# Kernel optimization log

Measured on AMD Instinct MI355X. Metric: run time of the kernel, lower is better.

Reference implementation:

```python
import jax, jax.numpy as jnp
import numpy as np

N, E, DIM, H = 50000, 800000, 64, 4

def setup_inputs() -> dict:
    key = jax.random.key(0)
    k0, k1, k2, k3, k4 = jax.random.split(key, 5)
    h_v = jax.random.normal(k0, (N, DIM), dtype=jnp.float32)
    src = jax.random.randint(k1, (E,), 0, N, dtype=jnp.int64)
    dst = jax.random.randint(k2, (E,), 0, N, dtype=jnp.int64)
    W_fc = jax.random.normal(k3, (DIM * H, DIM), dtype=jnp.float32) * 0.05
    b_fc = jnp.zeros((DIM * H,), dtype=jnp.float32)
    W_pi = jax.random.normal(k4, (1, DIM * H), dtype=jnp.float32) * 0.05
    return {"h_v": h_v, "src": src, "dst": dst, "W_fc": W_fc, "b_fc": b_fc, "W_pi": W_pi}

def reference(h_v, src, dst, W_fc, b_fc, W_pi):
    n, dim = h_v.shape
    heads = W_fc.shape[0] // dim
    # fc: [N, dim] -> [N, H*dim]
    ft = h_v @ W_fc.T + b_fc
    # u_mul_v: per-edge elementwise product of src/dst features  [E, H*dim]
    e = ft[src] * ft[dst]
    # pi + LeakyReLU(0.2): per-edge scalar score  [E]
    s = jax.nn.leaky_relu(e @ W_pi.T, negative_slope=0.2)[:, 0]
    # edge_softmax over incoming edges of each destination node (stable)
    smax = jax.ops.segment_max(s, dst, num_segments=n)
    ex = jnp.exp(s - smax[dst])
    denom = jax.ops.segment_sum(ex, dst, num_segments=n)
    a = ex / denom[dst]                        # [E]
    # u_mul_e + scatter-sum into destination nodes  [N, H*dim]
    agg = jax.ops.segment_sum(ft[src] * a[:, None], dst, num_segments=n)
    # max-pool over heads  [N, dim]
    return agg.reshape(n, heads, dim).max(axis=1)
```

## Files before the change

kernel.cpp:

```cpp
#include <hip/hip_runtime.h>
#include <math.h>

#define DIM 64
#define FDIM 256
#define MAXD 64
#define DEFER_THR 4.0f
#define XSTR 20

typedef _Float16 h2 __attribute__((ext_vector_type(2)));
typedef float f2 __attribute__((ext_vector_type(2)));

__global__ __launch_bounds__(256) void fc_kernel(const float* __restrict__ h,
                                                 const float* __restrict__ W,
                                                 const float* __restrict__ b,
                                                 _Float16* __restrict__ ft,
                                                 int* __restrict__ cnt, int N)
{
    for (int i = blockIdx.x * blockDim.x + threadIdx.x; i < N;
         i += gridDim.x * blockDim.x) cnt[i] = 0;

    int t = threadIdx.x;
    float w[DIM];
#pragma unroll
    for (int j = 0; j < DIM / 4; ++j) {
        float4 v = *(const float4*)(W + (size_t)t * DIM + j * 4);
        w[4 * j + 0] = v.x; w[4 * j + 1] = v.y;
        w[4 * j + 2] = v.z; w[4 * j + 3] = v.w;
    }
    float bt = b[t];
    for (int r = blockIdx.x; r < N; r += gridDim.x) {
        const float4* h4 = (const float4*)(h + (size_t)r * DIM);
        float acc = bt;
#pragma unroll
        for (int j = 0; j < DIM / 4; ++j) {
            float4 hv = h4[j];
            acc = fmaf(hv.x, w[4 * j + 0], acc);
            acc = fmaf(hv.y, w[4 * j + 1], acc);
            acc = fmaf(hv.z, w[4 * j + 2], acc);
            acc = fmaf(hv.w, w[4 * j + 3], acc);
        }
        ft[(size_t)r * FDIM + t] = (_Float16)acc;
    }
}

__global__ void bucket_kernel(const int* __restrict__ src, const int* __restrict__ dst,
                              int* __restrict__ cnt, unsigned short* __restrict__ egrid,
                              int E)
{
    int i = blockIdx.x * blockDim.x + threadIdx.x;
    if (i < E) {
        int d = dst[i];
        int slot = atomicAdd(&cnt[d], 1);
        egrid[(size_t)d * MAXD + slot] = (unsigned short)src[i];
    }
}

__global__ __launch_bounds__(256) void agg_kernel(const _Float16* __restrict__ ft,
                                                  const int* __restrict__ cnt,
                                                  const unsigned short* __restrict__ egrid,
                                                  const float* __restrict__ Wpi,
                                                  float* __restrict__ out, int N)
{
    __shared__ float xb[4][64 * XSTR];
    int wid = (blockIdx.x * blockDim.x + threadIdx.x) >> 6;
    int wv  = threadIdx.x >> 6;
    int lane = threadIdx.x & 63;
    if (wid >= N) return;
    int q  = lane >> 4;
    int ql = lane & 15;

    h2 fdwh[8];
    {
        const float* wp = Wpi + ql * 16;
        const _Float16* drow = ft + (size_t)wid * FDIM + ql * 16;
        uint4 a = *(const uint4*)(drow);
        uint4 b = *(const uint4*)(drow + 8);
        const h2* da = (const h2*)&a;
        const h2* db = (const h2*)&b;
#pragma unroll
        for (int j = 0; j < 4; ++j) {
            h2 v = da[j], u = db[j];
            fdwh[j].x     = (_Float16)((float)v.x * wp[2 * j + 0]);
            fdwh[j].y     = (_Float16)((float)v.y * wp[2 * j + 1]);
            fdwh[4 + j].x = (_Float16)((float)u.x * wp[8 + 2 * j + 0]);
            fdwh[4 + j].y = (_Float16)((float)u.y * wp[8 + 2 * j + 1]);
        }
    }

    int e0 = wid * MAXD;
    int e1 = e0 + cnt[wid];
    float mq = -INFINITY, lq = 0.f;
    f2 acc2[8];
#pragma unroll
    for (int j = 0; j < 8; ++j) acc2[j] = (f2){0.f, 0.f};

    auto IDX = [&](int it, int& s1, int& s2, bool& v1, bool& v2) {
        int lo = e0 + it * 8 + q, hi = e0 + it * 8 + q + 4;
        v1 = lo < e1; v2 = hi < e1;
        s1 = egrid[v1 ? lo : e0];
        s2 = egrid[v2 ? hi : e0];
    };
    auto ROWS = [&](int s1, int s2, uint4& a1, uint4& b1, uint4& a2, uint4& b2) {
        const _Float16* r1 = ft + (size_t)s1 * FDIM + ql * 16;
        const _Float16* r2 = ft + (size_t)s2 * FDIM + ql * 16;
        a1 = *(const uint4*)(r1);
        b1 = *(const uint4*)(r1 + 8);
        a2 = *(const uint4*)(r2);
        b2 = *(const uint4*)(r2 + 8);
    };
    auto COMP8 = [&](uint4 a1, uint4 b1, uint4 a2, uint4 b2, bool v1, bool v2) {
        const h2* fa1 = (const h2*)&a1; const h2* fb1 = (const h2*)&b1;
        const h2* fa2 = (const h2*)&a2; const h2* fb2 = (const h2*)&b2;
        float p1 = 0.f, p2 = 0.f;
#pragma unroll
        for (int j = 0; j < 4; ++j) {
            p1 = __builtin_amdgcn_fdot2(fa1[j], fdwh[j], p1, false);
            p2 = __builtin_amdgcn_fdot2(fa2[j], fdwh[j], p2, false);
        }
#pragma unroll
        for (int j = 0; j < 4; ++j) {
            p1 = __builtin_amdgcn_fdot2(fb1[j], fdwh[4 + j], p1, false);
            p2 = __builtin_amdgcn_fdot2(fb2[j], fdwh[4 + j], p2, false);
        }
        p1 += __shfl_xor(p1, 1, 64);  p2 += __shfl_xor(p2, 1, 64);
        p1 += __shfl_xor(p1, 2, 64);  p2 += __shfl_xor(p2, 2, 64);
        p1 += __shfl_xor(p1, 4, 64);  p2 += __shfl_xor(p2, 4, 64);
        p1 += __shfl_xor(p1, 8, 64);  p2 += __shfl_xor(p2, 8, 64);
        float s1 = p1 > 0.f ? p1 : 0.2f * p1;
        float s2 = p2 > 0.f ? p2 : 0.2f * p2;
        if (!v1) s1 = -INFINITY;
        if (!v2) s2 = -INFINITY;
        float smax = fmaxf(s1, s2);
        if (smax > mq + DEFER_THR) {
            float sc = __expf(mq - smax);
            lq *= sc;
            f2 sc2 = {sc, sc};
#pragma unroll
            for (int j = 0; j < 8; ++j) acc2[j] *= sc2;
            mq = smax;
        }
        float pe1 = v1 ? __expf(s1 - mq) : 0.f;
        float pe2 = v2 ? __expf(s2 - mq) : 0.f;
        lq += pe1 + pe2;
        f2 pe1v = {pe1, pe1}, pe2v = {pe2, pe2};
#pragma unroll
        for (int j = 0; j < 4; ++j) {
            f2 w1 = {(float)fa1[j].x, (float)fa1[j].y};
            f2 w2 = {(float)fa2[j].x, (float)fa2[j].y};
            acc2[j] = __builtin_elementwise_fma(pe1v, w1,
                       __builtin_elementwise_fma(pe2v, w2, acc2[j]));
            f2 u1 = {(float)fb1[j].x, (float)fb1[j].y};
            f2 u2 = {(float)fb2[j].x, (float)fb2[j].y};
            acc2[4 + j] = __builtin_elementwise_fma(pe1v, u1,
                           __builtin_elementwise_fma(pe2v, u2, acc2[4 + j]));
        }
    };

    if (e0 < e1) {
        int nit = (e1 - e0 + 7) >> 3;
        int iAs1, iAs2, iBs1, iBs2, iCs1, iCs2;
        bool vA1, vA2, vB1, vB2, vC1, vC2;
        uint4 Ra1, Rb1, Ra2, Rb2, Sa1, Sb1, Sa2, Sb2;
        IDX(0, iAs1, iAs2, vA1, vA2);
        if (nit > 1) IDX(1, iBs1, iBs2, vB1, vB2);
        ROWS(iAs1, iAs2, Ra1, Rb1, Ra2, Rb2);
        int it = 0;
        while (true) {
            if (it + 2 < nit) IDX(it + 2, iCs1, iCs2, vC1, vC2);
            if (it + 1 < nit) ROWS(iBs1, iBs2, Sa1, Sb1, Sa2, Sb2);
            COMP8(Ra1, Rb1, Ra2, Rb2, vA1, vA2);
            ++it; if (it >= nit) break;
            iAs1 = iBs1; iAs2 = iBs2; vA1 = vB1; vA2 = vB2;
            iBs1 = iCs1; iBs2 = iCs2; vB1 = vC1; vB2 = vC2;
            if (it + 2 < nit) IDX(it + 2, iCs1, iCs2, vC1, vC2);
            if (it + 1 < nit) ROWS(iBs1, iBs2, Ra1, Rb1, Ra2, Rb2);
            COMP8(Sa1, Sb1, Sa2, Sb2, vA1, vA2);
            ++it; if (it >= nit) break;
            iAs1 = iBs1; iAs2 = iBs2; vA1 = vB1; vA2 = vB2;
            iBs1 = iCs1; iBs2 = iCs2; vB1 = vC1; vB2 = vC2;
        }
    }

    float mstar = fmaxf(mq, __shfl_xor(mq, 16, 64));
    mstar = fmaxf(mstar, __shfl_xor(mstar, 32, 64));
    float sc = (lq > 0.f) ? __expf(mq - mstar) : 0.f;
    float lt = lq * sc;
    lt += __shfl_xor(lt, 16, 64);
    lt += __shfl_xor(lt, 32, 64);
    float inv = (lt > 0.f) ? 1.f / lt : 0.f;

    {
        float* wp = &xb[wv][(unsigned)lane * XSTR];
        f2 sc2 = {sc, sc};
#pragma unroll
        for (int k = 0; k < 4; ++k) {
            f2 lo = acc2[2 * k] * sc2;
            f2 hi = acc2[2 * k + 1] * sc2;
            *(float4*)(wp + 4 * k) = make_float4(lo.x, lo.y, hi.x, hi.y);
        }
    }
    asm volatile("s_waitcnt lgkmcnt(0)" ::: "memory");
    {
        int col = lane >> 4, jp = lane & 15;
        float A[4];
#pragma unroll
        for (int h = 0; h < 4; ++h) {
            int rowb = (col + 4 * h) * XSTR + jp;
            float v0 = xb[wv][rowb];
            float v1 = xb[wv][rowb + 16 * XSTR];
            float v2 = xb[wv][rowb + 32 * XSTR];
            float v3 = xb[wv][rowb + 48 * XSTR];
            A[h] = (v0 + v1) + (v2 + v3);
        }
        float r = fmaxf(fmaxf(A[0], A[1]), fmaxf(A[2], A[3])) * inv;
        out[(size_t)wid * DIM + lane] = r;
    }
}

extern "C" void kernel_launch(void* const* d_in, const int* in_sizes, int n_in,
                              void* d_out, int out_size, void* d_ws, size_t ws_size,
                              hipStream_t stream)
{
    const float* h_v  = (const float*)d_in[0];
    const int*   src  = (const int*)d_in[1];
    const int*   dst  = (const int*)d_in[2];
    const float* W_fc = (const float*)d_in[3];
    const float* b_fc = (const float*)d_in[4];
    const float* W_pi = (const float*)d_in[5];
    float* out = (float*)d_out;

    int N = in_sizes[0] / DIM;
    int E = in_sizes[1];

    _Float16* ft = (_Float16*)d_ws;
    size_t ftB = (((size_t)N * FDIM * 2) + 255) & ~(size_t)255;
    char*  p     = (char*)d_ws + ftB;
    int*   cnt   = (int*)(p);
    unsigned short* egrid = (unsigned short*)(p + 256 * 1024);

    int eb = (E + 255) / 256;
    fc_kernel<<<1024, 256, 0, stream>>>(h_v, W_fc, b_fc, ft, cnt, N);
    bucket_kernel<<<eb, 256, 0, stream>>>(src, dst, cnt, egrid, E);
    int blocks = (N * 64 + 255) / 256;
    agg_kernel<<<blocks, 256, 0, stream>>>(ft, cnt, egrid, W_pi, out, N);
}
```

Measured before the change: 151.4 us.

## Compute fc projection with fp16 MFMA instead of scalar FMA

Replaces the scalar per-thread dot-product fc kernel with an MFMA 16x16x32 f16 kernel. Each wavefront computes a 16-row tile across all 256 output columns, after a new prep kernel converts W to fp16 and zeroes the counters. The goal is to take the dense projection off the scalar FMA path. In exchange it adds a kernel launch, quantizes h and W to fp16 before the multiply, and only handles N divisible by 16, with no tail path for leftover rows.

```diff
diff --git a/kernel.cpp b/kernel.cpp
--- a/kernel.cpp
+++ b/kernel.cpp
@@ -8,38 +8,55 @@
 #define XSTR 20
 
 typedef _Float16 h2 __attribute__((ext_vector_type(2)));
+typedef _Float16 h8 __attribute__((ext_vector_type(8)));
 typedef float f2 __attribute__((ext_vector_type(2)));
-
-__global__ __launch_bounds__(256) void fc_kernel(const float* __restrict__ h,
-                                                 const float* __restrict__ W,
-                                                 const float* __restrict__ b,
-                                                 _Float16* __restrict__ ft,
-                                                 int* __restrict__ cnt, int N)
-{
-    for (int i = blockIdx.x * blockDim.x + threadIdx.x; i < N;
-         i += gridDim.x * blockDim.x) cnt[i] = 0;
-
-    int t = threadIdx.x;
-    float w[DIM];
-#pragma unroll
-    for (int j = 0; j < DIM / 4; ++j) {
-        float4 v = *(const float4*)(W + (size_t)t * DIM + j * 4);
-        w[4 * j + 0] = v.x; w[4 * j + 1] = v.y;
-        w[4 * j + 2] = v.z; w[4 * j + 3] = v.w;
-    }
-    float bt = b[t];
-    for (int r = blockIdx.x; r < N; r += gridDim.x) {
-        const float4* h4 = (const float4*)(h + (size_t)r * DIM);
-        float acc = bt;
-#pragma unroll
-        for (int j = 0; j < DIM / 4; ++j) {
-            float4 hv = h4[j];
-            acc = fmaf(hv.x, w[4 * j + 0], acc);
-            acc = fmaf(hv.y, w[4 * j + 1], acc);
-            acc = fmaf(hv.z, w[4 * j + 2], acc);
-            acc = fmaf(hv.w, w[4 * j + 3], acc);
-        }
-        ft[(size_t)r * FDIM + t] = (_Float16)acc;
+typedef float f4 __attribute__((ext_vector_type(4)));
+
+__global__ void prep_kernel(const float* __restrict__ W, _Float16* __restrict__ Wh,
+                            int* __restrict__ cnt, int N)
+{
+    int i = blockIdx.x * blockDim.x + threadIdx.x;
+    if (i < FDIM * DIM) Wh[i] = (_Float16)W[i];
+    if (i < N) cnt[i] = 0;
+}
+
+__global__ __launch_bounds__(256) void fc_mfma_kernel(const float* __restrict__ h,
+                                                      const _Float16* __restrict__ Wh,
+                                                      const float* __restrict__ b,
+                                                      _Float16* __restrict__ ft, int N)
+{
+    int gw = blockIdx.x * 4 + (threadIdx.x >> 6);
+    int lane = threadIdx.x & 63;
+    int nrt = N >> 4;
+    if (gw >= nrt) return;
+    int g = lane >> 4;
+    int c = lane & 15;
+
+    const float* hrow = h + (size_t)(gw * 16 + c) * DIM;
+    h8 af[2];
+#pragma unroll
+    for (int kk = 0; kk < 2; ++kk) {
+        float4 a0 = *(const float4*)(hrow + kk * 32 + g * 8);
+        float4 a1 = *(const float4*)(hrow + kk * 32 + g * 8 + 4);
+        af[kk][0] = (_Float16)a0.x; af[kk][1] = (_Float16)a0.y;
+        af[kk][2] = (_Float16)a0.z; af[kk][3] = (_Float16)a0.w;
+        af[kk][4] = (_Float16)a1.x; af[kk][5] = (_Float16)a1.y;
+        af[kk][6] = (_Float16)a1.z; af[kk][7] = (_Float16)a1.w;
+    }
+    int orow = gw * 16 + 4 * g;
+#pragma unroll 4
+    for (int ct = 0; ct < 16; ++ct) {
+        int col = ct * 16 + c;
+        float bt = b[col];
+        f4 acc = (f4){bt, bt, bt, bt};
+        const _Float16* wrow = Wh + (size_t)col * DIM;
+        h8 b0 = *(const h8*)(wrow + g * 8);
+        h8 b1 = *(const h8*)(wrow + 32 + g * 8);
+        acc = __builtin_amdgcn_mfma_f32_16x16x32_f16(af[0], b0, acc, 0, 0, 0);
+        acc = __builtin_amdgcn_mfma_f32_16x16x32_f16(af[1], b1, acc, 0, 0, 0);
+#pragma unroll
+        for (int r = 0; r < 4; ++r)
+            ft[(size_t)(orow + r) * FDIM + col] = (_Float16)acc[r];
     }
 }
 
@@ -237,9 +254,13 @@
     char*  p     = (char*)d_ws + ftB;
     int*   cnt   = (int*)(p);
     unsigned short* egrid = (unsigned short*)(p + 256 * 1024);
+    _Float16* Wh = (_Float16*)(p + 256 * 1024 + (size_t)50048 * MAXD * 2);
 
     int eb = (E + 255) / 256;
-    fc_kernel<<<1024, 256, 0, stream>>>(h_v, W_fc, b_fc, ft, cnt, N);
+    int nrt = N >> 4;
+    int fcb = (nrt + 3) / 4;
+    prep_kernel<<<(N + 255) / 256, 256, 0, stream>>>(W_fc, Wh, cnt, N);
+    fc_mfma_kernel<<<fcb, 256, 0, stream>>>(h_v, Wh, b_fc, ft, N);
     bucket_kernel<<<eb, 256, 0, stream>>>(src, dst, cnt, egrid, E);
     int blocks = (N * 64 + 255) / 256;
     agg_kernel<<<blocks, 256, 0, stream>>>(ft, cnt, egrid, W_pi, out, N);
```

New measurement: 139.1 us. 1.09x faster.
